# Optimization experiments

Measured on AMD Instinct MI355X. Metric: run time of the kernel, lower is better.

## Reference

```python
import jax, jax.numpy as jnp
import numpy as np

EPS = 1e-5

def _layernorm(x, gamma, beta):
    mu = jnp.mean(x, axis=-1, keepdims=True)
    var = jnp.mean(jnp.square(x - mu), axis=-1, keepdims=True)
    return (x - mu) * jax.lax.rsqrt(var + EPS) * gamma + beta

def setup_inputs() -> dict:
    key = jax.random.key(0)
    kx, kw = jax.random.split(key)
    N, D, BIT = 65536, 1024, 64
    X = jax.random.normal(kx, (N, D), dtype=jnp.float32)
    # xavier_uniform with gain=0.5 for weight [BIT, D]
    limit = 0.5 * np.sqrt(6.0 / (D + BIT))
    W = jax.random.uniform(kw, (BIT, D), minval=-limit, maxval=limit, dtype=jnp.float32)
    b = jnp.zeros((BIT,), dtype=jnp.float32)
    ln1_g = jnp.ones((D,), dtype=jnp.float32)
    ln1_b = jnp.zeros((D,), dtype=jnp.float32)
    ln2_g = jnp.ones((BIT,), dtype=jnp.float32)
    ln2_b = jnp.zeros((BIT,), dtype=jnp.float32)
    return {"X": X, "W": W, "b": b, "ln1_g": ln1_g, "ln1_b": ln1_b, "ln2_g": ln2_g, "ln2_b": ln2_b}

def reference(X, W, b, ln1_g, ln1_b, ln2_g, ln2_b):
    # LayerNorm -> Linear -> LayerNorm
    xn = _layernorm(X, ln1_g, ln1_b)                       # [N, D]
    logits = jnp.einsum('nd,bd->nb', xn, W) + b            # [N, BIT]
    logits = _layernorm(logits, ln2_g, ln2_b)
    # mean-center over batch, tanh, sign-binarize
    logits = logits - jnp.mean(logits, axis=0, keepdims=True)
    H = jnp.tanh(0.5 * logits)
    B = jnp.where(H >= 0.0, jnp.int8(1), jnp.int8(-1))
    return H, B
```

## Files before the change

kernel.cpp:

```cpp
#include <hip/hip_runtime.h>
#include <stdint.h>

#define N_ROWS 65536
#define D_IN   1024
#define NBIT   64
#define LN_EPS 1e-5f

typedef __attribute__((ext_vector_type(8))) _Float16 f16x8;
typedef __attribute__((ext_vector_type(4))) float f32x4;

__device__ __forceinline__ void gload_lds16(const void* g, void* l) {
    __builtin_amdgcn_global_load_lds(
        (const __attribute__((address_space(1))) uint32_t*)g,
        (__attribute__((address_space(3))) uint32_t*)l, 16, 0, 0);
}

__device__ __forceinline__ f32x4 mfma16(f16x8 a, f16x8 b, f32x4 c) {
    return __builtin_amdgcn_mfma_f32_16x16x32_f16(a, b, c, 0, 0, 0);
}

__device__ __forceinline__ void do_tstep(f32x4 x0, f32x4 x1,
        const _Float16* bhp, f32x4* acc_h, f32x4* acc_m, f32x4* acc_ll,
        float& sum, float& sumsq) {
    float xs[8] = {x0[0], x0[1], x0[2], x0[3], x1[0], x1[1], x1[2], x1[3]};
    f16x8 ahi, alo;
#pragma unroll
    for (int j = 0; j < 8; ++j) {
        float xv = xs[j];
        sum += xv;
        sumsq = fmaf(xv, xv, sumsq);
        _Float16 h = (_Float16)xv;
        ahi[j] = h;
        alo[j] = (_Float16)((xv - (float)h) * 2048.0f);
    }
#pragma unroll
    for (int nt = 0; nt < 4; ++nt) {
        f16x8 bh = *(const f16x8*)(bhp + nt * 512);
        f16x8 bl = *(const f16x8*)(bhp + 8192 + nt * 512);
        acc_h[nt]  = mfma16(ahi, bh, acc_h[nt]);
        acc_m[nt]  = mfma16(ahi, bl, acc_m[nt]);
        acc_m[nt]  = mfma16(alo, bh, acc_m[nt]);
        acc_ll[nt] = mfma16(alo, bl, acc_ll[nt]);
    }
}

__global__ void prep_kernel(const float* __restrict__ W, const float* __restrict__ bias,
                            const float* __restrict__ g1, const float* __restrict__ b1,
                            _Float16* __restrict__ whi, _Float16* __restrict__ wlo,
                            float* __restrict__ u, float* __restrict__ v) {
    int bit = blockIdx.x;
    int t   = threadIdx.x;
    int nt  = bit >> 4, bl = bit & 15;
    float su = 0.f, sv = 0.f;
    for (int d = t; d < D_IN; d += 256) {
        float w  = W[bit * D_IN + d];
        float gw = w * g1[d];
        su += gw;
        sv += w * b1[d];
        int kt = d >> 5, gg = (d >> 3) & 3, j = d & 7;
        size_t idx = (((size_t)(kt * 4 + nt)) * 64 + gg * 16 + bl) * 8 + j;
        _Float16 h = (_Float16)gw;
        whi[idx] = h;
        wlo[idx] = (_Float16)((gw - (float)h) * 2048.0f);
    }
    __shared__ float s1[256], s2[256];
    s1[t] = su; s2[t] = sv;
    __syncthreads();
    for (int off = 128; off > 0; off >>= 1) {
        if (t < off) { s1[t] += s1[t + off]; s2[t] += s2[t + off]; }
        __syncthreads();
    }
    if (t == 0) { u[bit] = s1[0]; v[bit] = s2[0] + bias[bit]; }
}

__global__ void __launch_bounds__(256) main_kernel(
        const float* __restrict__ X,
        const _Float16* __restrict__ whi, const _Float16* __restrict__ wlo,
        const float* __restrict__ u, const float* __restrict__ v,
        const float* __restrict__ g2, const float* __restrict__ b2,
        float* __restrict__ L, float* __restrict__ P) {
    __shared__ _Float16 lw[2][16384];
    int tid  = threadIdx.x;
    int wid  = tid >> 6, lane = tid & 63;
    int g    = lane >> 4, r16 = lane & 15;
    int row_base = blockIdx.x * 64 + wid * 16;

    const float* xrow = X + (size_t)(row_base + r16) * D_IN + g * 8;

    const _Float16* gsrc = ((wid & 2) ? wlo : whi) + (wid & 1) * 4096 + (size_t)lane * 8;
    const int ldst = ((wid & 2) ? 8192 : 0) + (wid & 1) * 4096;

#define STAGEW(cc, buf) do {                                                  \
        const _Float16* gs_ = gsrc + (size_t)(cc) * 8192;                     \
        _Float16* ld_ = &lw[buf][ldst];                                       \
        _Pragma("unroll")                                                     \
        for (int r = 0; r < 8; ++r)                                           \
            gload_lds16(gs_ + r * 512, ld_ + r * 512);                        \
    } while (0)

    f32x4 acc_h0[4], acc_h1[4], acc_m[4], acc_ll[4];
#pragma unroll
    for (int nt = 0; nt < 4; ++nt) {
        acc_h0[nt] = (f32x4){0.f, 0.f, 0.f, 0.f};
        acc_h1[nt] = (f32x4){0.f, 0.f, 0.f, 0.f};
        acc_m[nt]  = (f32x4){0.f, 0.f, 0.f, 0.f};
        acc_ll[nt] = (f32x4){0.f, 0.f, 0.f, 0.f};
    }
    float sum = 0.f, sumsq = 0.f;

    STAGEW(0, 0);
    __syncthreads();

    for (int c = 0; c < 8; ++c) {
        if (c < 7) STAGEW(c + 1, (c + 1) & 1);
        const float* xp = xrow + c * 128;
        f32x4 xv[8];
#pragma unroll
        for (int t2 = 0; t2 < 4; ++t2) {
            xv[2 * t2]     = *(const f32x4*)(xp + t2 * 32);
            xv[2 * t2 + 1] = *(const f32x4*)(xp + t2 * 32 + 4);
        }
        const _Float16* bhp = &lw[c & 1][0] + lane * 8;
#pragma unroll
        for (int t2 = 0; t2 < 4; ++t2) {
            do_tstep(xv[2 * t2], xv[2 * t2 + 1], bhp + t2 * 2048,
                     (t2 & 1) ? acc_h1 : acc_h0, acc_m, acc_ll, sum, sumsq);
        }
        __syncthreads();
    }

    sum   += __shfl_xor(sum, 16);   sum   += __shfl_xor(sum, 32);
    sumsq += __shfl_xor(sumsq, 16); sumsq += __shfl_xor(sumsq, 32);
    float mu   = sum * (1.f / 1024.f);
    float var  = sumsq * (1.f / 1024.f) - mu * mu;
    float rstd = rsqrtf(var + LN_EPS);

    float uv[4], vv[4], g2v[4], b2v[4];
#pragma unroll
    for (int nt = 0; nt < 4; ++nt) {
        int bitc = nt * 16 + r16;
        uv[nt] = u[bitc]; vv[nt] = v[bitc]; g2v[nt] = g2[bitc]; b2v[nt] = b2[bitc];
    }
    float mu_m[4], rs_m[4];
#pragma unroll
    for (int reg = 0; reg < 4; ++reg) {
        int m = g * 4 + reg;
        mu_m[reg] = __shfl(mu, m);
        rs_m[reg] = __shfl(rstd, m);
    }

    float lg[4][4];
#pragma unroll
    for (int nt = 0; nt < 4; ++nt)
#pragma unroll
        for (int reg = 0; reg < 4; ++reg) {
            float dot = (acc_h0[nt][reg] + acc_h1[nt][reg])
                      + acc_m[nt][reg] * (1.0f / 2048.0f)
                      + acc_ll[nt][reg] * (1.0f / 4194304.0f);
            lg[nt][reg] = rs_m[reg] * dot - rs_m[reg] * mu_m[reg] * uv[nt] + vv[nt];
        }

#pragma unroll
    for (int reg = 0; reg < 4; ++reg) {
        float s1 = lg[0][reg] + lg[1][reg] + lg[2][reg] + lg[3][reg];
        float s2 = lg[0][reg]*lg[0][reg] + lg[1][reg]*lg[1][reg]
                 + lg[2][reg]*lg[2][reg] + lg[3][reg]*lg[3][reg];
#pragma unroll
        for (int m = 1; m <= 8; m <<= 1) {
            s1 += __shfl_xor(s1, m);
            s2 += __shfl_xor(s2, m);
        }
        float mean = s1 * (1.f / 64.f);
        float va   = s2 * (1.f / 64.f) - mean * mean;
        float rs2  = rsqrtf(va + LN_EPS);
#pragma unroll
        for (int nt = 0; nt < 4; ++nt)
            lg[nt][reg] = (lg[nt][reg] - mean) * rs2 * g2v[nt] + b2v[nt];
    }

#pragma unroll
    for (int reg = 0; reg < 4; ++reg) {
        size_t row = (size_t)(row_base + g * 4 + reg);
#pragma unroll
        for (int nt = 0; nt < 4; ++nt)
            L[row * 64 + nt * 16 + r16] = lg[nt][reg];
    }

#pragma unroll
    for (int nt = 0; nt < 4; ++nt) {
        float cs = lg[nt][0] + lg[nt][1] + lg[nt][2] + lg[nt][3];
        cs += __shfl_xor(cs, 16);
        cs += __shfl_xor(cs, 32);
        if (g == 0)
            P[(size_t)(nt * 16 + r16) * 4096 + blockIdx.x * 4 + wid] = cs;
    }
#undef STAGEW
}

__global__ void reduce_kernel(const float* __restrict__ P, float* __restrict__ cm) {
    int bit = blockIdx.x, t = threadIdx.x;
    float s = 0.f;
    for (int p = t; p < 4096; p += 256) s += P[(size_t)bit * 4096 + p];
    __shared__ float sh[256];
    sh[t] = s;
    __syncthreads();
    for (int off = 128; off > 0; off >>= 1) {
        if (t < off) sh[t] += sh[t + off];
        __syncthreads();
    }
    if (t == 0) cm[bit] = sh[0] * (1.f / (float)N_ROWS);
}

__global__ void final_kernel(const float* __restrict__ L, const float* __restrict__ cm,
                             float* __restrict__ out) {
    __shared__ float cms[64];
    if (threadIdx.x < 64) cms[threadIdx.x] = cm[threadIdx.x];
    __syncthreads();
    const f32x4* L4 = (const f32x4*)L;
    f32x4* H4 = (f32x4*)out;
    f32x4* B4 = (f32x4*)(out + (size_t)N_ROWS * NBIT);
    int total = N_ROWS * NBIT / 4;
    for (int i = blockIdx.x * blockDim.x + threadIdx.x; i < total;
         i += gridDim.x * blockDim.x) {
        f32x4 x = L4[i];
        int bb = (i & 15) * 4;
        f32x4 h, bo;
#pragma unroll
        for (int j = 0; j < 4; ++j) {
            float y  = 0.5f * (x[j] - cms[bb + j]);
            float y2 = y * y;
            float poly = y * fmaf(y2, fmaf(y2, 2.f / 15.f, -1.f / 3.f), 1.f);
            float e  = __expf(2.f * y);
            float ef = 1.f - 2.f / (e + 1.f);
            float hv = (fabsf(y) < 0.5f) ? poly : ef;
            h[j]  = hv;
            bo[j] = hv >= 0.f ? 1.f : -1.f;
        }
        __builtin_nontemporal_store(h, &H4[i]);
        __builtin_nontemporal_store(bo, &B4[i]);
    }
}

extern "C" void kernel_launch(void* const* d_in, const int* in_sizes, int n_in,
                              void* d_out, int out_size, void* d_ws, size_t ws_size,
                              hipStream_t stream) {
    (void)in_sizes; (void)n_in; (void)out_size; (void)ws_size;
    const float* X  = (const float*)d_in[0];
    const float* W  = (const float*)d_in[1];
    const float* bb = (const float*)d_in[2];
    const float* g1 = (const float*)d_in[3];
    const float* b1 = (const float*)d_in[4];
    const float* g2 = (const float*)d_in[5];
    const float* b2 = (const float*)d_in[6];

    char* ws = (char*)d_ws;
    _Float16* whi = (_Float16*)ws;
    _Float16* wlo = (_Float16*)(ws + 131072);
    float* u  = (float*)(ws + 262144);
    float* v  = (float*)(ws + 266240);
    float* P  = (float*)(ws + 270336);
    float* cm = (float*)(ws + 270336 + 64 * 4096 * 4);

    float* out = (float*)d_out;
    float* L   = out + (size_t)N_ROWS * NBIT;

    prep_kernel<<<64, 256, 0, stream>>>(W, bb, g1, b1, whi, wlo, u, v);
    main_kernel<<<1024, 256, 0, stream>>>(X, whi, wlo, u, v, g2, b2, L, P);
    reduce_kernel<<<64, 256, 0, stream>>>(P, cm);
    final_kernel<<<2048, 256, 0, stream>>>(L, cm, out);
}
```

Measured before the change: 91.87 us.

## Switch main GEMM to 32x32x16 MFMA tiles with 128-row blocks

Replaces the 16x16x32 MFMA tiling with 32x32x16 MFMA instructions, so each wave handles 32 rows and each block 128 rows. The prep kernel's weight layout and the epilogue (LayerNorm2, partial column sums) are rewritten to match the new accumulator layout. The grid is halved and the partial-sum buffer shrinks accordingly. The intent is more reuse of each LDS weight fragment per MFMA and fewer blocks staging the same weights, at the cost of larger accumulators and more register pressure. It also sets a launch-bounds occupancy hint of two blocks.

```diff
diff --git a/kernel.cpp b/kernel.cpp
--- a/kernel.cpp
+++ b/kernel.cpp
@@ -6,8 +6,9 @@
 #define NBIT   64
 #define LN_EPS 1e-5f
 
-typedef __attribute__((ext_vector_type(8))) _Float16 f16x8;
-typedef __attribute__((ext_vector_type(4))) float f32x4;
+typedef __attribute__((ext_vector_type(8)))  _Float16 f16x8;
+typedef __attribute__((ext_vector_type(4)))  float f32x4;
+typedef __attribute__((ext_vector_type(16))) float f32x16;
 
 __device__ __forceinline__ void gload_lds16(const void* g, void* l) {
     __builtin_amdgcn_global_load_lds(
@@ -15,33 +16,8 @@
         (__attribute__((address_space(3))) uint32_t*)l, 16, 0, 0);
 }
 
-__device__ __forceinline__ f32x4 mfma16(f16x8 a, f16x8 b, f32x4 c) {
-    return __builtin_amdgcn_mfma_f32_16x16x32_f16(a, b, c, 0, 0, 0);
-}
-
-__device__ __forceinline__ void do_tstep(f32x4 x0, f32x4 x1,
-        const _Float16* bhp, f32x4* acc_h, f32x4* acc_m, f32x4* acc_ll,
-        float& sum, float& sumsq) {
-    float xs[8] = {x0[0], x0[1], x0[2], x0[3], x1[0], x1[1], x1[2], x1[3]};
-    f16x8 ahi, alo;
-#pragma unroll
-    for (int j = 0; j < 8; ++j) {
-        float xv = xs[j];
-        sum += xv;
-        sumsq = fmaf(xv, xv, sumsq);
-        _Float16 h = (_Float16)xv;
-        ahi[j] = h;
-        alo[j] = (_Float16)((xv - (float)h) * 2048.0f);
-    }
-#pragma unroll
-    for (int nt = 0; nt < 4; ++nt) {
-        f16x8 bh = *(const f16x8*)(bhp + nt * 512);
-        f16x8 bl = *(const f16x8*)(bhp + 8192 + nt * 512);
-        acc_h[nt]  = mfma16(ahi, bh, acc_h[nt]);
-        acc_m[nt]  = mfma16(ahi, bl, acc_m[nt]);
-        acc_m[nt]  = mfma16(alo, bh, acc_m[nt]);
-        acc_ll[nt] = mfma16(alo, bl, acc_ll[nt]);
-    }
+__device__ __forceinline__ f32x16 mfma32(f16x8 a, f16x8 b, f32x16 c) {
+    return __builtin_amdgcn_mfma_f32_32x32x16_f16(a, b, c, 0, 0, 0);
 }
 
 __global__ void prep_kernel(const float* __restrict__ W, const float* __restrict__ bias,
@@ -50,15 +26,17 @@
                             float* __restrict__ u, float* __restrict__ v) {
     int bit = blockIdx.x;
     int t   = threadIdx.x;
-    int nt  = bit >> 4, bl = bit & 15;
+    int nt  = bit >> 5, col = bit & 31;
     float su = 0.f, sv = 0.f;
     for (int d = t; d < D_IN; d += 256) {
         float w  = W[bit * D_IN + d];
         float gw = w * g1[d];
         su += gw;
         sv += w * b1[d];
-        int kt = d >> 5, gg = (d >> 3) & 3, j = d & 7;
-        size_t idx = (((size_t)(kt * 4 + nt)) * 64 + gg * 16 + bl) * 8 + j;
+        int tg = d >> 4, c = tg >> 3, tt = tg & 7;
+        int hi = (d >> 3) & 1, j = d & 7;
+        int lane = col + 32 * hi;
+        size_t idx = (size_t)c * 8192 + tt * 1024 + nt * 512 + lane * 8 + j;
         _Float16 h = (_Float16)gw;
         whi[idx] = h;
         wlo[idx] = (_Float16)((gw - (float)h) * 2048.0f);
@@ -73,7 +51,7 @@
     if (t == 0) { u[bit] = s1[0]; v[bit] = s2[0] + bias[bit]; }
 }
 
-__global__ void __launch_bounds__(256) main_kernel(
+__global__ void __launch_bounds__(256, 2) main_kernel(
         const float* __restrict__ X,
         const _Float16* __restrict__ whi, const _Float16* __restrict__ wlo,
         const float* __restrict__ u, const float* __restrict__ v,
@@ -82,10 +60,10 @@
     __shared__ _Float16 lw[2][16384];
     int tid  = threadIdx.x;
     int wid  = tid >> 6, lane = tid & 63;
-    int g    = lane >> 4, r16 = lane & 15;
-    int row_base = blockIdx.x * 64 + wid * 16;
-
-    const float* xrow = X + (size_t)(row_base + r16) * D_IN + g * 8;
+    int col  = lane & 31, hi = lane >> 5;
+    int row_base = blockIdx.x * 128 + wid * 32;
+
+    const float* xrow = X + (size_t)(row_base + col) * D_IN + hi * 8;
 
     const _Float16* gsrc = ((wid & 2) ? wlo : whi) + (wid & 1) * 4096 + (size_t)lane * 8;
     const int ldst = ((wid & 2) ? 8192 : 0) + (wid & 1) * 4096;
@@ -98,13 +76,11 @@
             gload_lds16(gs_ + r * 512, ld_ + r * 512);                        \
     } while (0)
 
-    f32x4 acc_h0[4], acc_h1[4], acc_m[4], acc_ll[4];
-#pragma unroll
-    for (int nt = 0; nt < 4; ++nt) {
-        acc_h0[nt] = (f32x4){0.f, 0.f, 0.f, 0.f};
-        acc_h1[nt] = (f32x4){0.f, 0.f, 0.f, 0.f};
-        acc_m[nt]  = (f32x4){0.f, 0.f, 0.f, 0.f};
-        acc_ll[nt] = (f32x4){0.f, 0.f, 0.f, 0.f};
+    f32x16 aH0[2], aH1[2], aM[2], aLL[2];
+#pragma unroll
+    for (int nt = 0; nt < 2; ++nt) {
+        aH0[nt] = (f32x16)(0.f); aH1[nt] = (f32x16)(0.f);
+        aM[nt]  = (f32x16)(0.f); aLL[nt] = (f32x16)(0.f);
     }
     float sum = 0.f, sumsq = 0.f;
 
@@ -114,85 +90,91 @@
     for (int c = 0; c < 8; ++c) {
         if (c < 7) STAGEW(c + 1, (c + 1) & 1);
         const float* xp = xrow + c * 128;
-        f32x4 xv[8];
-#pragma unroll
-        for (int t2 = 0; t2 < 4; ++t2) {
-            xv[2 * t2]     = *(const f32x4*)(xp + t2 * 32);
-            xv[2 * t2 + 1] = *(const f32x4*)(xp + t2 * 32 + 4);
-        }
-        const _Float16* bhp = &lw[c & 1][0] + lane * 8;
-#pragma unroll
-        for (int t2 = 0; t2 < 4; ++t2) {
-            do_tstep(xv[2 * t2], xv[2 * t2 + 1], bhp + t2 * 2048,
-                     (t2 & 1) ? acc_h1 : acc_h0, acc_m, acc_ll, sum, sumsq);
+        const _Float16* lwb = &lw[c & 1][0] + lane * 8;
+#pragma unroll
+        for (int t = 0; t < 8; ++t) {
+            f32x4 x0 = *(const f32x4*)(xp + t * 16);
+            f32x4 x1 = *(const f32x4*)(xp + t * 16 + 4);
+            float xs[8] = {x0[0], x0[1], x0[2], x0[3], x1[0], x1[1], x1[2], x1[3]};
+            f16x8 ahi, alo;
+#pragma unroll
+            for (int j = 0; j < 8; ++j) {
+                float xv = xs[j];
+                sum += xv;
+                sumsq = fmaf(xv, xv, sumsq);
+                _Float16 h = (_Float16)xv;
+                ahi[j] = h;
+                alo[j] = (_Float16)((xv - (float)h) * 2048.0f);
+            }
+            const _Float16* base = lwb + t * 1024;
+#pragma unroll
+            for (int nt = 0; nt < 2; ++nt) {
+                f16x8 bh = *(const f16x8*)(base + nt * 512);
+                f16x8 bl = *(const f16x8*)(base + nt * 512 + 8192);
+                if (t & 1) aH1[nt] = mfma32(ahi, bh, aH1[nt]);
+                else       aH0[nt] = mfma32(ahi, bh, aH0[nt]);
+                aM[nt]  = mfma32(ahi, bl, aM[nt]);
+                aM[nt]  = mfma32(alo, bh, aM[nt]);
+                aLL[nt] = mfma32(alo, bl, aLL[nt]);
+            }
         }
         __syncthreads();
     }
 
-    sum   += __shfl_xor(sum, 16);   sum   += __shfl_xor(sum, 32);
-    sumsq += __shfl_xor(sumsq, 16); sumsq += __shfl_xor(sumsq, 32);
+    sum   += __shfl_xor(sum, 32);
+    sumsq += __shfl_xor(sumsq, 32);
     float mu   = sum * (1.f / 1024.f);
     float var  = sumsq * (1.f / 1024.f) - mu * mu;
     float rstd = rsqrtf(var + LN_EPS);
 
-    float uv[4], vv[4], g2v[4], b2v[4];
-#pragma unroll
-    for (int nt = 0; nt < 4; ++nt) {
-        int bitc = nt * 16 + r16;
+    float uv[2], vv[2], g2v[2], b2v[2];
+#pragma unroll
+    for (int nt = 0; nt < 2; ++nt) {
+        int bitc = nt * 32 + col;
         uv[nt] = u[bitc]; vv[nt] = v[bitc]; g2v[nt] = g2[bitc]; b2v[nt] = b2[bitc];
     }
-    float mu_m[4], rs_m[4];
-#pragma unroll
-    for (int reg = 0; reg < 4; ++reg) {
-        int m = g * 4 + reg;
-        mu_m[reg] = __shfl(mu, m);
-        rs_m[reg] = __shfl(rstd, m);
-    }
-
-    float lg[4][4];
-#pragma unroll
-    for (int nt = 0; nt < 4; ++nt)
-#pragma unroll
-        for (int reg = 0; reg < 4; ++reg) {
-            float dot = (acc_h0[nt][reg] + acc_h1[nt][reg])
-                      + acc_m[nt][reg] * (1.0f / 2048.0f)
-                      + acc_ll[nt][reg] * (1.0f / 4194304.0f);
-            lg[nt][reg] = rs_m[reg] * dot - rs_m[reg] * mu_m[reg] * uv[nt] + vv[nt];
-        }
-
-#pragma unroll
-    for (int reg = 0; reg < 4; ++reg) {
-        float s1 = lg[0][reg] + lg[1][reg] + lg[2][reg] + lg[3][reg];
-        float s2 = lg[0][reg]*lg[0][reg] + lg[1][reg]*lg[1][reg]
-                 + lg[2][reg]*lg[2][reg] + lg[3][reg]*lg[3][reg];
-#pragma unroll
-        for (int m = 1; m <= 8; m <<= 1) {
+
+    float ps0 = 0.f, ps1 = 0.f;
+#pragma unroll
+    for (int reg = 0; reg < 16; ++reg) {
+        int r = (reg & 3) + 8 * (reg >> 2) + 4 * hi;
+        float mu_r = __shfl(mu, r);
+        float rs_r = __shfl(rstd, r);
+        float lg0, lg1;
+        {
+            float d0 = (aH0[0][reg] + aH1[0][reg])
+                     + aM[0][reg] * (1.0f / 2048.0f)
+                     + aLL[0][reg] * (1.0f / 4194304.0f);
+            float d1 = (aH0[1][reg] + aH1[1][reg])
+                     + aM[1][reg] * (1.0f / 2048.0f)
+                     + aLL[1][reg] * (1.0f / 4194304.0f);
+            lg0 = rs_r * d0 - rs_r * mu_r * uv[0] + vv[0];
+            lg1 = rs_r * d1 - rs_r * mu_r * uv[1] + vv[1];
+        }
+        float s1 = lg0 + lg1;
+        float s2 = lg0 * lg0 + lg1 * lg1;
+#pragma unroll
+        for (int m = 1; m <= 16; m <<= 1) {
             s1 += __shfl_xor(s1, m);
             s2 += __shfl_xor(s2, m);
         }
         float mean = s1 * (1.f / 64.f);
         float va   = s2 * (1.f / 64.f) - mean * mean;
         float rs2  = rsqrtf(va + LN_EPS);
-#pragma unroll
-        for (int nt = 0; nt < 4; ++nt)
-            lg[nt][reg] = (lg[nt][reg] - mean) * rs2 * g2v[nt] + b2v[nt];
-    }
-
-#pragma unroll
-    for (int reg = 0; reg < 4; ++reg) {
-        size_t row = (size_t)(row_base + g * 4 + reg);
-#pragma unroll
-        for (int nt = 0; nt < 4; ++nt)
-            L[row * 64 + nt * 16 + r16] = lg[nt][reg];
-    }
-
-#pragma unroll
-    for (int nt = 0; nt < 4; ++nt) {
-        float cs = lg[nt][0] + lg[nt][1] + lg[nt][2] + lg[nt][3];
-        cs += __shfl_xor(cs, 16);
-        cs += __shfl_xor(cs, 32);
-        if (g == 0)
-            P[(size_t)(nt * 16 + r16) * 4096 + blockIdx.x * 4 + wid] = cs;
+        float o0 = (lg0 - mean) * rs2 * g2v[0] + b2v[0];
+        float o1 = (lg1 - mean) * rs2 * g2v[1] + b2v[1];
+        size_t row = (size_t)(row_base + r);
+        L[row * 64 + col]      = o0;
+        L[row * 64 + 32 + col] = o1;
+        ps0 += o0;
+        ps1 += o1;
+    }
+
+    ps0 += __shfl_xor(ps0, 32);
+    ps1 += __shfl_xor(ps1, 32);
+    if (hi == 0) {
+        P[(size_t)col * 2048        + blockIdx.x * 4 + wid] = ps0;
+        P[(size_t)(32 + col) * 2048 + blockIdx.x * 4 + wid] = ps1;
     }
 #undef STAGEW
 }
@@ -200,7 +182,7 @@
 __global__ void reduce_kernel(const float* __restrict__ P, float* __restrict__ cm) {
     int bit = blockIdx.x, t = threadIdx.x;
     float s = 0.f;
-    for (int p = t; p < 4096; p += 256) s += P[(size_t)bit * 4096 + p];
+    for (int p = t; p < 2048; p += 256) s += P[(size_t)bit * 2048 + p];
     __shared__ float sh[256];
     sh[t] = s;
     __syncthreads();
@@ -259,13 +241,13 @@
     float* u  = (float*)(ws + 262144);
     float* v  = (float*)(ws + 266240);
     float* P  = (float*)(ws + 270336);
-    float* cm = (float*)(ws + 270336 + 64 * 4096 * 4);
+    float* cm = (float*)(ws + 270336 + 64 * 2048 * 4);
 
     float* out = (float*)d_out;
     float* L   = out + (size_t)N_ROWS * NBIT;
 
     prep_kernel<<<64, 256, 0, stream>>>(W, bb, g1, b1, whi, wlo, u, v);
-    main_kernel<<<1024, 256, 0, stream>>>(X, whi, wlo, u, v, g2, b2, L, P);
+    main_kernel<<<512, 256, 0, stream>>>(X, whi, wlo, u, v, g2, b2, L, P);
     reduce_kernel<<<64, 256, 0, stream>>>(P, cm);
     final_kernel<<<2048, 256, 0, stream>>>(L, cm, out);
 }
```

Measured after the change: 84.39 us. 1.09x faster.
